# Kernel tuning notes

Hardware: AMD Instinct MI355X
Metric: run time of the kernel (lower is better)

Reference implementation:

```python
import jax, jax.numpy as jnp
import numpy as np

EPS = 1e-12  # VERY_SMALL_NUMBER
LN_EPS = 1e-5
N, NFEAT, NHID, A, P, HOPS = 50000, 256, 128, 32, 4, 2


def setup_inputs() -> dict:
    key = jax.random.key(0)
    ks = jax.random.split(key, 16)
    def w(i, shape, scale=0.05):
        return jax.random.normal(ks[i], shape, dtype=jnp.float32) * scale
    return {
        "x": jax.random.normal(ks[0], (N, NFEAT), dtype=jnp.float32),
        # input_mapper: Linear(nfeat,nhid) -> ReLU -> Linear(nhid,nhid)
        "im_w1": w(1, (NFEAT, NHID)), "im_b1": jnp.zeros((NHID,), jnp.float32),
        "im_w2": w(2, (NHID, NHID)),  "im_b2": jnp.zeros((NHID,), jnp.float32),
        # AnchorGraphLearner
        "anchors": w(3, (A, NHID), 1.0),
        "ml_w1": w(4, (P, 2 * NHID, NHID)), "ml_b1": jnp.zeros((P, NHID), jnp.float32),
        "ml_w2": w(5, (P, NHID)),            "ml_b2": jnp.zeros((P,), jnp.float32),
        # AnchorGNNLayer weights (xavier in torch; scaled randn here)
        "enc_w": w(6, (HOPS, NHID, NHID)), "enc_b": jnp.zeros((HOPS, NHID), jnp.float32),
        # LayerNorm
        "ln_g": jnp.ones((NHID,), jnp.float32), "ln_b": jnp.zeros((NHID,), jnp.float32),
        # classifier: Linear -> PReLU(nhid) -> Linear(nhid,2)
        "cls_w1": w(7, (NHID, NHID)), "cls_b1": jnp.zeros((NHID,), jnp.float32),
        "prelu_a": jnp.full((NHID,), 0.25, jnp.float32),
        "cls_w2": w(8, (NHID, 2)),   "cls_b2": jnp.zeros((2,), jnp.float32),
    }


def _forward(x, im_w1, im_b1, im_w2, im_b2, anchors, ml_w1, ml_b1, ml_w2, ml_b2,
             enc_w, enc_b, ln_g, ln_b, cls_w1, cls_b1, prelu_a, cls_w2, cls_b2):
    nhid = im_w2.shape[-1]
    # input_mapper (dropout is identity in eval)
    h = jnp.maximum(x @ im_w1 + im_b1, 0.0) @ im_w2 + im_b2  # [N, nhid]
    x_loc = h

    # --- AnchorGraphLearner: fused form of cat([x_i, a_j]) @ W1 ---
    Wx, Wa = ml_w1[:, :nhid, :], ml_w1[:, nhid:, :]  # each [P, nhid, nhid]
    attn = jnp.zeros((h.shape[0], anchors.shape[0]), h.dtype)
    for p in range(ml_w1.shape[0]):  # small fixed head count
        hx = h @ Wx[p]                               # [N, nhid]
        ha = anchors @ Wa[p]                         # [A, nhid]
        hid = jnp.maximum(hx[:, None, :] + ha[None, :, :] + ml_b1[p], 0.0)  # [N, A, nhid]
        attn = attn + jax.nn.sigmoid(hid @ ml_w2[p] + ml_b2[p])            # [N, A]
    adj = attn / ml_w1.shape[0]  # mean over heads, [N, A]

    # --- AnchorGNNLayer stack (anchor_mp normalized double matmul) ---
    node_norm = adj / jnp.maximum(adj.sum(axis=0, keepdims=True), EPS)     # col-normalized [N, A]
    anchor_norm = adj / jnp.maximum(adj.sum(axis=1, keepdims=True), EPS)   # row-normalized [N, A]
    xc = h
    for i in range(enc_w.shape[0]):
        support = xc @ enc_w[i]                          # [N, nhid]
        agg = node_norm.T @ support                      # [A, nhid]
        xc = jnp.maximum(anchor_norm @ agg + enc_b[i], 0.0)

    # residual + LayerNorm
    z = xc + x_loc
    mu = z.mean(axis=-1, keepdims=True)
    var = ((z - mu) ** 2).mean(axis=-1, keepdims=True)
    z = (z - mu) * jax.lax.rsqrt(var + LN_EPS) * ln_g + ln_b

    def classifier(t):
        t1 = t @ cls_w1 + cls_b1
        t1 = jnp.where(t1 > 0, t1, prelu_a * t1)  # PReLU(nhid)
        return t1 @ cls_w2 + cls_b2

    pred = classifier(z)                 # [N, 2]
    anchor_logits = classifier(anchors)  # [A, 2]
    anchor_vec = anchors[None]           # [1, A, nhid] (matches unsqueeze(0))
    return (pred, z, anchor_vec, anchor_logits)


def reference(x, im_w1, im_b1, im_w2, im_b2, anchors, ml_w1, ml_b1, ml_w2, ml_b2,
              enc_w, enc_b, ln_g, ln_b, cls_w1, cls_b1, prelu_a, cls_w2, cls_b2):
    return _forward(x, im_w1, im_b1, im_w2, im_b2, anchors, ml_w1, ml_b1, ml_w2, ml_b2,
                    enc_w, enc_b, ln_g, ln_b, cls_w1, cls_b1, prelu_a, cls_w2, cls_b2)
```

## Files before the change

kernel.cpp:

```cpp
#include <hip/hip_runtime.h>
#include <math.h>

#define NN 50000
#define FEAT 256
#define HID 128
#define NA 32
#define NP 4
#define TM 64
#define NBLK 782
#define NB2 781
#define LDA 132
#define EPSS 1e-12f
#define LN_EPS 1e-5f

typedef unsigned short u16;
typedef __attribute__((ext_vector_type(8))) short bf16x8;
typedef __attribute__((ext_vector_type(4))) float f32x4;

#define ADJ_F   0
#define RS_F    1600000
#define CS_F    1650000
#define AGG0_F  1650032
#define AGG1_F  1654128
#define HB_F    1658256
#define FLAG_F  1674640
#define F_END   1674672
#define XC_U   (2 * F_END)
#define SUP_U  (XC_U + NN * HID)
#define PW_U   (SUP_U + NN * HID)
#define PW_TOT 165638
#define WS_NEED_BYTES ((size_t)(PW_U + PW_TOT) * 2ULL)
#define CSP_OFF 0

#define PK_IMW1T  0
#define PK_IMW2T  32768
#define PK_MLW1T  49152
#define PK_ENCWT  114688
#define PK_CLSW1T 147456
#define PK_IMB1   163840
#define PK_IMB2   163968
#define PK_MLW2   164096
#define PK_ENCB   164608
#define PK_LNG    164864
#define PK_LNB    164992
#define PK_CLSB1  165120
#define PK_PRELU  165248
#define PK_CLSW2  165376
#define PK_CLSB2  165632
#define PK_MLB2   165634
#define PK_TOTAL  165638

#define PRED_OFF 0
#define Z_OFF    100000
#define AV_OFF   6500000
#define AL_OFF   6504096
#define OUT_TOT  6504160

__device__ __constant__ int kNel[19] = {
    NN * FEAT, FEAT * HID, HID, HID * HID, HID, NA * HID,
    NP * 2 * HID * HID, NP * HID, NP * HID, NP, 2 * HID * HID, 2 * HID,
    HID, HID, HID * HID, HID, HID, HID * 2, 2};

#define TSEG_TOT 163840
__device__ __constant__ int tLen[9]  = {32768,16384,16384,16384,16384,16384,16384,16384,16384};
__device__ __constant__ int tDst[9]  = {PK_IMW1T,PK_IMW2T,PK_MLW1T,PK_MLW1T+16384,
                                        PK_MLW1T+32768,PK_MLW1T+49152,PK_ENCWT,
                                        PK_ENCWT+16384,PK_CLSW1T};
__device__ __constant__ int tSrcT[9] = {1,3,6,6,6,6,10,10,14};
__device__ __constant__ int tBase[9] = {0,0,0,32768,65536,98304,0,16384,0};
#define VSEG_TOT 1798
__device__ __constant__ int vLen[11] = {128,128,512,256,128,128,128,128,256,2,4};
__device__ __constant__ int vDst[11] = {PK_IMB1,PK_IMB2,PK_MLW2,PK_ENCB,PK_LNG,PK_LNB,
                                        PK_CLSB1,PK_PRELU,PK_CLSW2,PK_CLSB2,PK_MLB2};
__device__ __constant__ int vSrcT[11]= {2,4,8,11,12,13,15,16,17,18,9};

struct P19 { const void* q[19]; };

__device__ __forceinline__ float b2f(u16 u) {
    union { float f; unsigned int i; } v; v.i = ((unsigned int)u) << 16; return v.f;
}
__device__ __forceinline__ u16 f2b(float f) {
    union { float f; unsigned int i; } v; v.f = f;
    unsigned int x = v.i;
    x += 0x7fffu + ((x >> 16) & 1u);
    return (u16)(x >> 16);
}
__device__ __forceinline__ float ldf(const void* p, size_t i, int fl) {
    if (fl == 1) return ((const float*)p)[i];
    if (fl == 0) return b2f(((const u16*)p)[i]);
    return 0.f;
}

__global__ __launch_bounds__(256) void k_detect_all(P19 a, int* __restrict__ flags) {
    __shared__ int sHi[256], sE[256], sO[256];
    const int b = blockIdx.x;
    const u16* p = (const u16*)a.q[b];
    const int M = (kNel[b] < 8192) ? kNel[b] : 8192;
    int cHi = 0, cE = 0, cO = 0;
    for (int j = threadIdx.x; j < M; j += 256) {
        const u16 v = p[j];
        if (j & 1) cO += (v != 0);
        else { cE += (v != 0); cHi += (((v >> 7) & 0xFF) >= 200); }
    }
    sHi[threadIdx.x] = cHi; sE[threadIdx.x] = cE; sO[threadIdx.x] = cO;
    __syncthreads();
    for (int s = 128; s > 0; s >>= 1) {
        if (threadIdx.x < (unsigned)s) {
            sHi[threadIdx.x] += sHi[threadIdx.x + s];
            sE[threadIdx.x]  += sE[threadIdx.x + s];
            sO[threadIdx.x]  += sO[threadIdx.x + s];
        }
        __syncthreads();
    }
    if (threadIdx.x == 0) {
        int f;
        if (sE[0] == 0 && sO[0] == 0) f = 2;
        else if (sHi[0] >= 4 || sE[0] == 0) f = 1;
        else f = 0;
        flags[b] = f;
    }
}

__global__ __launch_bounds__(256) void k_convT(P19 a, const int* __restrict__ flags,
                                               u16* __restrict__ pw) {
    int idx = blockIdx.x * 256 + threadIdx.x;
    if (idx >= TSEG_TOT) return;
    int off = idx, s = 0;
    while (off >= tLen[s]) { off -= tLen[s]; ++s; }
    int n, k;
    if (s == 0) { n = off >> 8; k = off & 255; }
    else        { n = off >> 7; k = off & 127; }
    const int si = tSrcT[s];
    pw[tDst[s] + off] = f2b(ldf(a.q[si], (size_t)tBase[s] + (size_t)k * 128 + n,
                                flags[si]));
}

__global__ __launch_bounds__(256) void k_convV(P19 a, const int* __restrict__ flags,
                                               u16* __restrict__ pw) {
    for (int idx = threadIdx.x; idx < VSEG_TOT; idx += 256) {
        int off = idx, s = 0;
        while (off >= vLen[s]) { off -= vLen[s]; ++s; }
        const int si = vSrcT[s];
        pw[vDst[s] + off] = f2b(ldf(a.q[si], off, flags[si]));
    }
}

__device__ __forceinline__ void mfma_64x128(const u16* As, const u16* Bt,
                                            f32x4 acc[8], int lane, int rowBase) {
    const int lr = lane & 15, lq = lane >> 4;
#pragma unroll
    for (int kc = 0; kc < 4; ++kc) {
        bf16x8 a = *(const bf16x8*)(As + (rowBase + lr) * 136 + kc * 32 + lq * 8);
#pragma unroll
        for (int t = 0; t < 8; ++t) {
            bf16x8 b = *(const bf16x8*)(Bt + (t * 16 + lr) * 136 + kc * 32 + lq * 8);
            acc[t] = __builtin_amdgcn_mfma_f32_16x16x32_bf16(a, b, acc[t], 0, 0, 0);
        }
    }
}

__global__ __launch_bounds__(256) void k_gemm2(const void* __restrict__ A,
                                               const u16* __restrict__ pw,
                                               float* __restrict__ outh,
                                               const int* __restrict__ flags) {
    __shared__ __align__(16) u16 As[64 * 136];
    __shared__ __align__(16) u16 Bt[128 * 136];
    const int fA = flags[0];
    const int tid = threadIdx.x;
    const int row0 = blockIdx.x * TM;
    const int lane = tid & 63, wv = tid >> 6, rowBase = wv * 16;
    const int lr = lane & 15, lq = lane >> 4;
    f32x4 acc[8];
    const f32x4 z4 = {0.f, 0.f, 0.f, 0.f};
#pragma unroll
    for (int t = 0; t < 8; ++t) acc[t] = z4;

    for (int kc = 0; kc < 2; ++kc) {
        for (int i = tid; i < 64 * 32; i += 256) {
            const int m = i >> 5, k4 = (i & 31) << 2;
            const int g = row0 + m;
            ushort4 o; o.x = 0; o.y = 0; o.z = 0; o.w = 0;
            if (g < NN) {
                const size_t idx = (size_t)g * FEAT + kc * 128 + k4;
                if (fA == 1) {
                    float4 v = *(const float4*)((const float*)A + idx);
                    o.x = f2b(v.x); o.y = f2b(v.y); o.z = f2b(v.z); o.w = f2b(v.w);
                } else {
                    o = *(const ushort4*)((const u16*)A + idx);
                }
            }
            *(ushort4*)&As[m * 136 + k4] = o;
        }
        for (int i = tid; i < 128 * 32; i += 256) {
            const int n = i >> 5, k4 = (i & 31) << 2;
            *(ushort4*)&Bt[n * 136 + k4] =
                *(const ushort4*)(pw + PK_IMW1T + (size_t)n * FEAT + kc * 128 + k4);
        }
        __syncthreads();
        mfma_64x128(As, Bt, acc, lane, rowBase);
        __syncthreads();
    }
#pragma unroll
    for (int t = 0; t < 8; ++t) {
        const int col = t * 16 + lr;
        const float bv = b2f(pw[PK_IMB1 + col]);
#pragma unroll
        for (int r = 0; r < 4; ++r)
            As[(rowBase + lq * 4 + r) * 136 + col] = f2b(fmaxf(acc[t][r] + bv, 0.f));
    }
    for (int i = tid; i < 128 * 32; i += 256) {
        const int n = i >> 5, k4 = (i & 31) << 2;
        *(ushort4*)&Bt[n * 136 + k4] =
            *(const ushort4*)(pw + PK_IMW2T + (size_t)n * HID + k4);
    }
    __syncthreads();
    f32x4 acc2[8];
#pragma unroll
    for (int t = 0; t < 8; ++t) acc2[t] = z4;
    mfma_64x128(As, Bt, acc2, lane, rowBase);
#pragma unroll
    for (int t = 0; t < 8; ++t) {
        const int col = t * 16 + lr;
        const float bv = b2f(pw[PK_IMB2 + col]);
#pragma unroll
        for (int r = 0; r < 4; ++r) {
            const int g = row0 + rowBase + lq * 4 + r;
            if (g < NN) outh[(size_t)g * HID + col] = acc2[t][r] + bv;
        }
    }
}

__global__ __launch_bounds__(128) void k_pre(const void* __restrict__ anchors,
                                             const void* __restrict__ ml_w1,
                                             const void* __restrict__ ml_b1,
                                             float* __restrict__ hb,
                                             const int* __restrict__ flags) {
    __shared__ float sa[HID];
    const int fAn = flags[5], fW1 = flags[6], fB1 = flags[7];
    const int p = blockIdx.x >> 5, a = blockIdx.x & 31, k = threadIdx.x;
    sa[k] = ldf(anchors, a * HID + k, fAn);
    __syncthreads();
    float acc = ldf(ml_b1, p * HID + k, fB1);
    const size_t wbase = ((size_t)p * 2 * HID + HID) * HID + k;
#pragma unroll 4
    for (int j = 0; j < HID; ++j)
        acc += sa[j] * ldf(ml_w1, wbase + (size_t)j * HID, fW1);
    hb[p * (NA * HID) + k * NA + a] = acc;
}

__global__ __launch_bounds__(128) void k_wc(const float* __restrict__ hb,
                                            const u16* __restrict__ pw,
                                            float* __restrict__ wc) {
    __shared__ float red[128];
    const int p = blockIdx.x, tid = threadIdx.x;
    const int a = tid & 31, q = tid >> 5;
    float s = 0.f;
    for (int k = q * 32; k < q * 32 + 32; ++k)
        s += b2f(pw[PK_MLW2 + p * HID + k]) * hb[(size_t)p * (NA * HID) + k * NA + a];
    red[tid] = 0.5f * s;
    __syncthreads();
    if (tid < 32)
        wc[p * NA + tid] = red[tid] + red[tid + 32] + red[tid + 64] + red[tid + 96];
}

__global__ __launch_bounds__(256) void k_anchor(const void* __restrict__ anchors,
                                                const void* __restrict__ cls_w1,
                                                const void* __restrict__ cls_b1,
                                                const void* __restrict__ prelu_a,
                                                const void* __restrict__ cls_w2,
                                                const void* __restrict__ cls_b2,
                                                float* __restrict__ out,
                                                const int* __restrict__ flags) {
    __shared__ float sa[2][HID];
    __shared__ float st1[2][HID];
    const int fAn = flags[5], fW1 = flags[14], fB1 = flags[15];
    const int fPa = flags[16], fW2 = flags[17], fB2 = flags[18];
    const int tid = threadIdx.x;
    const int a0 = blockIdx.x * 2;
    const int half = tid >> 7, k = tid & 127;
    sa[half][k] = ldf(anchors, (a0 + half) * HID + k, fAn);
    __syncthreads();
    float acc = ldf(cls_b1, k, fB1);
#pragma unroll 4
    for (int j = 0; j < HID; ++j) acc += sa[half][j] * ldf(cls_w1, j * HID + k, fW1);
    const float pa = ldf(prelu_a, k, fPa);
    st1[half][k] = acc > 0.f ? acc : pa * acc;
    __syncthreads();
    if (tid < 4) {
        const int aa = tid >> 1, c = tid & 1;
        float s = ldf(cls_b2, c, fB2);
        for (int j = 0; j < HID; ++j) s += st1[aa][j] * ldf(cls_w2, j * 2 + c, fW2);
        out[AL_OFF + (a0 + aa) * 2 + c] = s;
    }
    if (blockIdx.x == 0) {
        for (int i = tid; i < NA * HID; i += 256)
            out[AV_OFF + i] = ldf(anchors, i, fAn);
    }
}

__global__ __launch_bounds__(256) void k_fattn(const float* __restrict__ h,
                                               const u16* __restrict__ pw,
                                               const float* __restrict__ hb,
                                               const float* __restrict__ wc,
                                               float* __restrict__ adj,
                                               float* __restrict__ rowsum,
                                               float* __restrict__ csPart) {
    __shared__ __align__(16) u16 Bt[128 * 136];
    __shared__ float hws[HID];
    __shared__ float wcs[NA];
    __shared__ float swr[4][NA];
    float* hbf = (float*)&Bt[64 * 136];
    const int tid = threadIdx.x;
    const int row0 = blockIdx.x * TM;
    const int lane = tid & 63, wv = tid >> 6, rowBase = wv * 16;
    const int lr = lane & 15, lq = lane >> 4;
    const int g = tid & 3, myrow = tid >> 2;
    const int a0 = g * 8;

    bf16x8 afr[4];
    {
        const int gr = row0 + rowBase + lr;
#pragma unroll
        for (int kc = 0; kc < 4; ++kc) {
            bf16x8 t;
            if (gr < NN) {
                const float* src = h + (size_t)gr * HID + kc * 32 + lq * 8;
                float4 v0 = *(const float4*)src;
                float4 v1 = *(const float4*)(src + 4);
                t[0] = (short)f2b(v0.x); t[1] = (short)f2b(v0.y);
                t[2] = (short)f2b(v0.z); t[3] = (short)f2b(v0.w);
                t[4] = (short)f2b(v1.x); t[5] = (short)f2b(v1.y);
                t[6] = (short)f2b(v1.z); t[7] = (short)f2b(v1.w);
            } else {
#pragma unroll
                for (int j = 0; j < 8; ++j) t[j] = 0;
            }
            afr[kc] = t;
        }
    }

    float adjacc[8];
#pragma unroll
    for (int j = 0; j < 8; ++j) adjacc[j] = 0.f;

    for (int p = 0; p < NP; ++p) {
        __syncthreads();
        for (int i = tid; i < 128 * 32; i += 256) {
            const int n = i >> 5, k4 = (i & 31) << 2;
            *(ushort4*)&Bt[n * 136 + k4] =
                *(const ushort4*)(pw + PK_MLW1T + p * 16384 + n * 128 + k4);
        }
        float4 hbreg[4];
        {
            const float4* hbp4 = (const float4*)(hb + (size_t)p * (NA * HID));
#pragma unroll
            for (int j = 0; j < 4; ++j) hbreg[j] = hbp4[tid + j * 256];
        }
        if (tid < HID) hws[tid] = 0.5f * b2f(pw[PK_MLW2 + p * HID + tid]);
        if (tid < NA) wcs[tid] = wc[p * NA + tid];
        __syncthreads();

        f32x4 acc[8];
        const f32x4 z4 = {0.f, 0.f, 0.f, 0.f};
#pragma unroll
        for (int t = 0; t < 8; ++t) acc[t] = z4;
#pragma unroll
        for (int kc = 0; kc < 4; ++kc)
#pragma unroll
            for (int t = 0; t < 8; ++t) {
                bf16x8 b = *(const bf16x8*)(Bt + (t * 16 + lr) * 136 + kc * 32 + lq * 8);
                acc[t] = __builtin_amdgcn_mfma_f32_16x16x32_bf16(afr[kc], b, acc[t], 0, 0, 0);
            }
        __syncthreads();
#pragma unroll
        for (int t = 0; t < 8; ++t)
#pragma unroll
            for (int r = 0; r < 4; ++r)
                Bt[(rowBase + lq * 4 + r) * 136 + t * 16 + lr] = f2b(acc[t][r]);
#pragma unroll
        for (int j = 0; j < 4; ++j)
            ((float4*)hbf)[tid + j * 256] = hbreg[j];
        __syncthreads();

        const float b2v = b2f(pw[PK_MLB2 + p]);
        float sabs[8], wh = 0.f;
#pragma unroll
        for (int j = 0; j < 8; ++j) sabs[j] = 0.f;

#pragma unroll 4
        for (int kp = 0; kp < 64; ++kp) {
            const unsigned hx2 = *(const unsigned*)&Bt[myrow * 136 + kp * 2];
            union { unsigned u; float f; } u0, u1;
            u0.u = hx2 << 16;
            u1.u = hx2 & 0xffff0000u;
            const float f0 = u0.f, f1 = u1.f;
            const float2 hw2 = *(const float2*)&hws[kp * 2];
            wh = fmaf(hw2.x, f0, wh);
            wh = fmaf(hw2.y, f1, wh);
            const float4 c00 = *(const float4*)&hbf[(kp * 2) * NA + a0];
            const float4 c01 = *(const float4*)&hbf[(kp * 2) * NA + a0 + 4];
            const float4 c10 = *(const float4*)&hbf[(kp * 2 + 1) * NA + a0];
            const float4 c11 = *(const float4*)&hbf[(kp * 2 + 1) * NA + a0 + 4];
            sabs[0] = fmaf(hw2.x, fabsf(f0 + c00.x), sabs[0]);
            sabs[1] = fmaf(hw2.x, fabsf(f0 + c00.y), sabs[1]);
            sabs[2] = fmaf(hw2.x, fabsf(f0 + c00.z), sabs[2]);
            sabs[3] = fmaf(hw2.x, fabsf(f0 + c00.w), sabs[3]);
            sabs[4] = fmaf(hw2.x, fabsf(f0 + c01.x), sabs[4]);
            sabs[5] = fmaf(hw2.x, fabsf(f0 + c01.y), sabs[5]);
            sabs[6] = fmaf(hw2.x, fabsf(f0 + c01.z), sabs[6]);
            sabs[7] = fmaf(hw2.x, fabsf(f0 + c01.w), sabs[7]);
            sabs[0] = fmaf(hw2.y, fabsf(f1 + c10.x), sabs[0]);
            sabs[1] = fmaf(hw2.y, fabsf(f1 + c10.y), sabs[1]);
            sabs[2] = fmaf(hw2.y, fabsf(f1 + c10.z), sabs[2]);
            sabs[3] = fmaf(hw2.y, fabsf(f1 + c10.w), sabs[3]);
            sabs[4] = fmaf(hw2.y, fabsf(f1 + c11.x), sabs[4]);
            sabs[5] = fmaf(hw2.y, fabsf(f1 + c11.y), sabs[5]);
            sabs[6] = fmaf(hw2.y, fabsf(f1 + c11.z), sabs[6]);
            sabs[7] = fmaf(hw2.y, fabsf(f1 + c11.w), sabs[7]);
        }
#pragma unroll
        for (int j = 0; j < 8; ++j) {
            const float s = wh + wcs[a0 + j] + b2v + sabs[j];
            adjacc[j] += 0.25f / (1.f + __expf(-s));
        }
    }

    const int grow = row0 + myrow;
    if (grow >= NN) {
#pragma unroll
        for (int j = 0; j < 8; ++j) adjacc[j] = 0.f;
    }
    if (grow < NN) {
        float* dst = adj + (size_t)grow * NA + a0;
        *(float4*)dst = make_float4(adjacc[0], adjacc[1], adjacc[2], adjacc[3]);
        *(float4*)(dst + 4) = make_float4(adjacc[4], adjacc[5], adjacc[6], adjacc[7]);
    }
    float rs = 0.f;
#pragma unroll
    for (int j = 0; j < 8; ++j) rs += adjacc[j];
    rs += __shfl_xor(rs, 1);
    rs += __shfl_xor(rs, 2);
    if (g == 0 && grow < NN) rowsum[grow] = rs;
#pragma unroll
    for (int st = 4; st <= 32; st <<= 1)
#pragma unroll
        for (int j = 0; j < 8; ++j) adjacc[j] += __shfl_xor(adjacc[j], st);
    if (lane < 4) {
#pragma unroll
        for (int j = 0; j < 8; ++j) swr[wv][lane * 8 + j] = adjacc[j];
    }
    __syncthreads();
    if (tid < NA)
        csPart[tid * NBLK + blockIdx.x] =
            swr[0][tid] + swr[1][tid] + swr[2][tid] + swr[3][tid];
}

__global__ __launch_bounds__(256) void k_cs_red(const float* __restrict__ csPart,
                                                float* __restrict__ colsum) {
    __shared__ float red[256];
    const int a = blockIdx.x, tid = threadIdx.x;
    float s = 0.f;
    for (int b = tid; b < NBLK; b += 256) s += csPart[a * NBLK + b];
    red[tid] = s;
    __syncthreads();
    for (int st = 128; st > 0; st >>= 1) {
        if (tid < st) red[tid] += red[tid + st];
        __syncthreads();
    }
    if (tid == 0) colsum[a] = red[0];
}

__global__ __launch_bounds__(256) void k_aggT(const float* __restrict__ adj,
                                              const float* __restrict__ h,
                                              float* __restrict__ part) {
    __shared__ float sT[TM][LDA];
    __shared__ float adjT[TM][NA + 1];
    const int tid = threadIdx.x;
    const int a0 = (tid & 15) * 2, k0 = (tid >> 4) * 8;
    float acc[2][8];
#pragma unroll
    for (int ia = 0; ia < 2; ++ia)
#pragma unroll
        for (int j = 0; j < 8; ++j) acc[ia][j] = 0.f;

    const int nt = (blockIdx.x == NB2 - 1) ? 2 : 1;
    for (int t = 0; t < nt; ++t) {
        const int row0 = (blockIdx.x + t) * TM;
        __syncthreads();
        for (int i = tid; i < TM * 32; i += 256) {
            const int m = i >> 5, k4 = (i & 31) << 2, g = row0 + m;
            float4 v = make_float4(0.f, 0.f, 0.f, 0.f);
            if (g < NN) v = *(const float4*)(h + (size_t)g * HID + k4);
            *(float4*)&sT[m][k4] = v;
        }
        for (int i = tid; i < TM * NA; i += 256) {
            const int m = i >> 5, a = i & 31, g = row0 + m;
            adjT[m][a] = (g < NN) ? adj[(size_t)g * NA + a] : 0.f;
        }
        __syncthreads();
#pragma unroll 4
        for (int n = 0; n < TM; ++n) {
            const float a0v = adjT[n][a0], a1v = adjT[n][a0 + 1];
            float4 s0 = *(const float4*)&sT[n][k0];
            float4 s1 = *(const float4*)&sT[n][k0 + 4];
            float sv[8] = {s0.x, s0.y, s0.z, s0.w, s1.x, s1.y, s1.z, s1.w};
#pragma unroll
            for (int j = 0; j < 8; ++j) {
                acc[0][j] += a0v * sv[j];
                acc[1][j] += a1v * sv[j];
            }
        }
    }
    float* dst = part + (size_t)blockIdx.x * (NA * HID);
#pragma unroll
    for (int ia = 0; ia < 2; ++ia) {
        *(float4*)&dst[(a0 + ia) * HID + k0] =
            make_float4(acc[ia][0], acc[ia][1], acc[ia][2], acc[ia][3]);
        *(float4*)&dst[(a0 + ia) * HID + k0 + 4] =
            make_float4(acc[ia][4], acc[ia][5], acc[ia][6], acc[ia][7]);
    }
}

__global__ __launch_bounds__(256) void k_Tred(const float* __restrict__ part,
                                              float* __restrict__ T) {
    __shared__ float red[256];
    const int jj = threadIdx.x & 15, bq = threadIdx.x >> 4;
    const int j = blockIdx.x * 16 + jj;
    float s = 0.f;
#pragma unroll 8
    for (int b = bq; b < NB2; b += 16) s += part[(size_t)b * (NA * HID) + j];
    red[threadIdx.x] = s;
    __syncthreads();
    if (bq == 0) {
        float t = 0.f;
#pragma unroll
        for (int q = 0; q < 16; ++q) t += red[q * 16 + jj];
        T[j] = t;
    }
}

__global__ __launch_bounds__(128) void k_small(const float* __restrict__ T,
                                               const u16* __restrict__ pw,
                                               const int hop,
                                               float* __restrict__ agg) {
    __shared__ float tr[HID];
    const int a = blockIdx.x, n = threadIdx.x;
    tr[n] = T[a * HID + n];
    __syncthreads();
    const u16* w = pw + PK_ENCWT + hop * HID * HID + n * HID;
    float s = 0.f;
#pragma unroll 4
    for (int j4 = 0; j4 < HID; j4 += 4) {
        ushort4 u = *(const ushort4*)(w + j4);
        s += tr[j4] * b2f(u.x) + tr[j4 + 1] * b2f(u.y) +
             tr[j4 + 2] * b2f(u.z) + tr[j4 + 3] * b2f(u.w);
    }
    agg[a * HID + n] = s;
}

__global__ __launch_bounds__(256) void k_e2a(const float* __restrict__ adj,
                                             const float* __restrict__ rowsum,
                                             const float* __restrict__ colsum,
                                             const float* __restrict__ agg,
                                             const u16* __restrict__ pw,
                                             float* __restrict__ part) {
    __shared__ float aggn[NA][LDA];
    __shared__ float adjT[TM][NA + 1];
    __shared__ __align__(8) u16 xcs[TM * 136];
    __shared__ float csl[NA], rsl[TM];
    const int tid = threadIdx.x;
    const int n0 = (tid & 31) * 4, m0 = (tid >> 5) * 8;
    const int a0 = (tid & 15) * 2, k0 = (tid >> 4) * 8;

    if (tid < NA) csl[tid] = fmaxf(colsum[tid], EPSS);
    __syncthreads();
    for (int i = tid; i < (NA * HID) / 4; i += 256) {
        const int a = i >> 5, k4 = (i & 31) << 2;
        float4 v = *(const float4*)(agg + a * HID + k4);
        const float inv = 1.f / csl[a];
        v.x *= inv; v.y *= inv; v.z *= inv; v.w *= inv;
        *(float4*)&aggn[a][k4] = v;
    }
    float bv[4];
#pragma unroll
    for (int j = 0; j < 4; ++j) bv[j] = b2f(pw[PK_ENCB + n0 + j]);

    float acc2[2][8];
#pragma unroll
    for (int ia = 0; ia < 2; ++ia)
#pragma unroll
        for (int j = 0; j < 8; ++j) acc2[ia][j] = 0.f;

    const int nt = (blockIdx.x == NB2 - 1) ? 2 : 1;
    for (int t = 0; t < nt; ++t) {
        const int row0 = (blockIdx.x + t) * TM;
        __syncthreads();
        for (int i = tid; i < TM * NA; i += 256) {
            const int m = i >> 5, a = i & 31, g = row0 + m;
            adjT[m][a] = (g < NN) ? adj[(size_t)g * NA + a] : 0.f;
        }
        if (tid >= 64 && tid < 128) {
            const int m = tid - 64, g = row0 + m;
            rsl[m] = (g < NN) ? 1.f / fmaxf(rowsum[g], EPSS) : 0.f;
        }
        __syncthreads();
        float acc[8][4];
#pragma unroll
        for (int i = 0; i < 8; ++i)
#pragma unroll
            for (int j = 0; j < 4; ++j) acc[i][j] = 0.f;
        for (int a = 0; a < NA; ++a) {
            float4 gv = *(const float4*)&aggn[a][n0];
            float gvv[4] = {gv.x, gv.y, gv.z, gv.w};
#pragma unroll
            for (int i = 0; i < 8; ++i) {
                const float av = adjT[m0 + i][a];
#pragma unroll
                for (int j = 0; j < 4; ++j) acc[i][j] += av * gvv[j];
            }
        }
#pragma unroll
        for (int i = 0; i < 8; ++i) {
            const float r = rsl[m0 + i];
            ushort4 o;
            o.x = f2b(fmaxf(r * acc[i][0] + bv[0], 0.f));
            o.y = f2b(fmaxf(r * acc[i][1] + bv[1], 0.f));
            o.z = f2b(fmaxf(r * acc[i][2] + bv[2], 0.f));
            o.w = f2b(fmaxf(r * acc[i][3] + bv[3], 0.f));
            *(ushort4*)&xcs[(m0 + i) * 136 + n0] = o;
        }
        __syncthreads();
#pragma unroll 4
        for (int n = 0; n < TM; ++n) {
            const float a0v = adjT[n][a0], a1v = adjT[n][a0 + 1];
            ushort4 u0 = *(const ushort4*)&xcs[n * 136 + k0];
            ushort4 u1 = *(const ushort4*)&xcs[n * 136 + k0 + 4];
            float sv[8] = {b2f(u0.x), b2f(u0.y), b2f(u0.z), b2f(u0.w),
                           b2f(u1.x), b2f(u1.y), b2f(u1.z), b2f(u1.w)};
#pragma unroll
            for (int j = 0; j < 8; ++j) {
                acc2[0][j] += a0v * sv[j];
                acc2[1][j] += a1v * sv[j];
            }
        }
    }
    float* dst = part + (size_t)blockIdx.x * (NA * HID);
#pragma unroll
    for (int ia = 0; ia < 2; ++ia) {
        *(float4*)&dst[(a0 + ia) * HID + k0] =
            make_float4(acc2[ia][0], acc2[ia][1], acc2[ia][2], acc2[ia][3]);
        *(float4*)&dst[(a0 + ia) * HID + k0 + 4] =
            make_float4(acc2[ia][4], acc2[ia][5], acc2[ia][6], acc2[ia][7]);
    }
}

__global__ __launch_bounds__(256) void k_e2f(const float* __restrict__ adj,
                                             const float* __restrict__ rowsum,
                                             const float* __restrict__ colsum,
                                             const float* __restrict__ agg,
                                             const u16* __restrict__ pw,
                                             float* __restrict__ out) {
    __shared__ __align__(16) u16 As[64 * 136];
    __shared__ __align__(16) u16 uniB[128 * 136];
    __shared__ float smu[TM], sinv[TM], sg[HID], sb[HID], w2s[2 * HID];
    __shared__ float csl[NA], rsl[TM];
    float* aggn  = (float*)As;
    float* adjTf = (float*)uniB;
    float* zT    = (float*)uniB;
    const int tid = threadIdx.x;
    const int row0 = blockIdx.x * TM;
    const int lane = tid & 63, wv = tid >> 6, rowBase = wv * 16;
    const int lr = lane & 15, lq = lane >> 4;
    const int n0 = (tid & 31) * 4, m0 = (tid >> 5) * 8;
    const float* h = out + Z_OFF;

    if (tid < NA) csl[tid] = fmaxf(colsum[tid], EPSS);
    if (tid >= 64 && tid < 128) {
        const int m = tid - 64, g = row0 + m;
        rsl[m] = (g < NN) ? 1.f / fmaxf(rowsum[g], EPSS) : 0.f;
    }
    for (int i = tid; i < TM * NA; i += 256) {
        const int m = i >> 5, a = i & 31, g = row0 + m;
        adjTf[m * (NA + 1) + a] = (g < NN) ? adj[(size_t)g * NA + a] : 0.f;
    }
    __syncthreads();
    for (int i = tid; i < (NA * HID) / 4; i += 256) {
        const int a = i >> 5, k4 = (i & 31) << 2;
        float4 v = *(const float4*)(agg + a * HID + k4);
        const float inv = 1.f / csl[a];
        v.x *= inv; v.y *= inv; v.z *= inv; v.w *= inv;
        *(float4*)&aggn[a * LDA + k4] = v;
    }
    __syncthreads();
    float acc[8][4];
#pragma unroll
    for (int i = 0; i < 8; ++i)
#pragma unroll
        for (int j = 0; j < 4; ++j) acc[i][j] = 0.f;
    for (int a = 0; a < NA; ++a) {
        float4 gv = *(const float4*)&aggn[a * LDA + n0];
        float gvv[4] = {gv.x, gv.y, gv.z, gv.w};
#pragma unroll
        for (int i = 0; i < 8; ++i) {
            const float av = adjTf[(m0 + i) * (NA + 1) + a];
#pragma unroll
            for (int j = 0; j < 4; ++j) acc[i][j] += av * gvv[j];
        }
    }
    float bv[4];
#pragma unroll
    for (int j = 0; j < 4; ++j) bv[j] = b2f(pw[PK_ENCB + HID + n0 + j]);
    float xcv[8][4];
#pragma unroll
    for (int i = 0; i < 8; ++i) {
        const float r = rsl[m0 + i];
#pragma unroll
        for (int j = 0; j < 4; ++j)
            xcv[i][j] = fmaxf(r * acc[i][j] + bv[j], 0.f);
    }
    __syncthreads();
#pragma unroll
    for (int i = 0; i < 8; ++i) {
        const int g = row0 + m0 + i;
        float4 hv = make_float4(0.f, 0.f, 0.f, 0.f);
        if (g < NN) hv = *(const float4*)(h + (size_t)g * HID + n0);
        float4 zv = make_float4(xcv[i][0] + hv.x, xcv[i][1] + hv.y,
                                xcv[i][2] + hv.z, xcv[i][3] + hv.w);
        *(float4*)&zT[(m0 + i) * 132 + n0] = zv;
    }
    if (tid < HID) { sg[tid] = b2f(pw[PK_LNG + tid]); sb[tid] = b2f(pw[PK_LNB + tid]); }
    w2s[tid] = b2f(pw[PK_CLSW2 + tid]);
    __syncthreads();
    if (tid < TM) {
        float s = 0.f;
        for (int k = 0; k < HID; ++k) s += zT[tid * 132 + k];
        const float mu = s * (1.f / HID);
        float v = 0.f;
        for (int k = 0; k < HID; ++k) { const float d = zT[tid * 132 + k] - mu; v += d * d; }
        smu[tid] = mu;
        sinv[tid] = rsqrtf(v * (1.f / HID) + LN_EPS);
    }
    __syncthreads();
    for (int i = tid; i < TM * 32; i += 256) {
        const int m = i >> 5, k4 = (i & 31) << 2, g = row0 + m;
        float4 v = *(const float4*)&zT[m * 132 + k4];
        const float mu = smu[m], inv = sinv[m];
        v.x = (v.x - mu) * inv * sg[k4 + 0] + sb[k4 + 0];
        v.y = (v.y - mu) * inv * sg[k4 + 1] + sb[k4 + 1];
        v.z = (v.z - mu) * inv * sg[k4 + 2] + sb[k4 + 2];
        v.w = (v.w - mu) * inv * sg[k4 + 3] + sb[k4 + 3];
        if (g < NN) *(float4*)&out[Z_OFF + (size_t)g * HID + k4] = v;
        ushort4 o; o.x = f2b(v.x); o.y = f2b(v.y); o.z = f2b(v.z); o.w = f2b(v.w);
        *(ushort4*)&As[m * 136 + k4] = o;
    }
    __syncthreads();
    for (int i = tid; i < 128 * 32; i += 256) {
        const int n = i >> 5, k4 = (i & 31) << 2;
        *(ushort4*)&uniB[n * 136 + k4] =
            *(const ushort4*)(pw + PK_CLSW1T + n * 128 + k4);
    }
    __syncthreads();
    f32x4 macc[8];
    const f32x4 z4 = {0.f, 0.f, 0.f, 0.f};
#pragma unroll
    for (int t = 0; t < 8; ++t) macc[t] = z4;
    mfma_64x128(As, uniB, macc, lane, rowBase);
    __syncthreads();
#pragma unroll
    for (int t = 0; t < 8; ++t) {
        const int col = t * 16 + lr;
        const float bc = b2f(pw[PK_CLSB1 + col]);
        const float pa = b2f(pw[PK_PRELU + col]);
#pragma unroll
        for (int r = 0; r < 4; ++r) {
            float v = macc[t][r] + bc;
            v = v > 0.f ? v : pa * v;
            As[(rowBase + lq * 4 + r) * 136 + col] = f2b(v);
        }
    }
    __syncthreads();
    if (tid < 128) {
        const int r = tid >> 1, c = tid & 1, g = row0 + r;
        if (g < NN) {
            float s = b2f(pw[PK_CLSB2 + c]);
            for (int k = 0; k < HID; ++k) s += b2f(As[r * 136 + k]) * w2s[k * 2 + c];
            out[PRED_OFF + (size_t)g * 2 + c] = s;
        }
    }
}

extern "C" void kernel_launch(void* const* d_in, const int* in_sizes, int n_in,
                              void* d_out, int out_size, void* d_ws, size_t ws_size,
                              hipStream_t stream) {
    const bool ok = (n_in >= 19) && (out_size == OUT_TOT) &&
                    (ws_size >= WS_NEED_BYTES) &&
                    (in_sizes[0] == NN * FEAT) && (in_sizes[6] == NP * 2 * HID * HID) &&
                    (in_sizes[10] == 2 * HID * HID) && (in_sizes[17] == HID * 2);
    if (!ok) {
        hipMemsetAsync(d_out, 0, (size_t)OUT_TOT * 4, stream);
        return;
    }

    float* ws    = (float*)d_ws;
    u16*   wsu   = (u16*)d_ws;
    float* out   = (float*)d_out;
    int*   flags = (int*)(ws + FLAG_F);
    float* hbuf  = out + Z_OFF;
    u16*   pw    = wsu + PW_U;
    float* xcf   = (float*)(wsu + XC_U);
    float* csPart = xcf + CSP_OFF;
    float* partb = (float*)(wsu + SUP_U);
    float* Tbuf  = ws + HB_F;
    float* wcv   = ws + AGG1_F;

    P19 pa;
    for (int i = 0; i < 19; ++i) pa.q[i] = d_in[i];
    k_detect_all<<<19, 256, 0, stream>>>(pa, flags);
    k_convT<<<(TSEG_TOT + 255) / 256, 256, 0, stream>>>(pa, flags, pw);
    k_convV<<<1, 256, 0, stream>>>(pa, flags, pw);

    k_pre<<<NP * NA, 128, 0, stream>>>(d_in[5], d_in[6], d_in[7], ws + HB_F, flags);
    k_wc<<<NP, 128, 0, stream>>>(ws + HB_F, pw, wcv);
    k_anchor<<<NA / 2, 256, 0, stream>>>(d_in[5], d_in[14], d_in[15], d_in[16],
                                         d_in[17], d_in[18], out, flags);

    k_gemm2<<<NBLK, 256, 0, stream>>>(d_in[0], pw, hbuf, flags);

    k_fattn<<<NBLK, 256, 0, stream>>>(hbuf, pw, ws + HB_F, wcv, ws + ADJ_F,
                                      ws + RS_F, csPart);
    k_cs_red<<<NA, 256, 0, stream>>>(csPart, ws + CS_F);

    k_aggT<<<NB2, 256, 0, stream>>>(ws + ADJ_F, hbuf, partb);
    k_Tred<<<256, 256, 0, stream>>>(partb, Tbuf);
    k_small<<<NA, 128, 0, stream>>>(Tbuf, pw, 0, ws + AGG0_F);
    k_e2a<<<NB2, 256, 0, stream>>>(ws + ADJ_F, ws + RS_F, ws + CS_F, ws + AGG0_F,
                                   pw, partb);
    k_Tred<<<256, 256, 0, stream>>>(partb, Tbuf);
    k_small<<<NA, 128, 0, stream>>>(Tbuf, pw, 1, ws + AGG1_F);
    k_e2f<<<NBLK, 256, 0, stream>>>(ws + ADJ_F, ws + RS_F, ws + CS_F, ws + AGG1_F,
                                    pw, out);
}
```

Before: 446.4 us.

## Fuse adjacency-transpose aggregation into attention kernel and drop separate aggT pass

The adj^T·h partial aggregation is now computed at the end of k_fattn. It reuses the bf16 h fragments already held in registers and the adjacency values already computed, staged through shared memory, so the separate k_aggT kernel no longer re-reads adj and h from global memory. The hb buffer prefetch is moved from registers to a direct global-to-LDS copy after the MFMA phase, which lowers register pressure. k_e2a and k_Tred now use one 64-row tile per block over 782 blocks instead of giving the last block two tiles. The fused aggregation uses bf16-rounded h where k_aggT used fp32 h, which slightly changes precision, and it adds tail work and a barrier to the attention kernel.

```diff
diff --git a/kernel.cpp b/kernel.cpp
--- a/kernel.cpp
+++ b/kernel.cpp
@@ -8,7 +8,6 @@
 #define NP 4
 #define TM 64
 #define NBLK 782
-#define NB2 781
 #define LDA 132
 #define EPSS 1e-12f
 #define LN_EPS 1e-5f
@@ -30,7 +29,6 @@
 #define PW_U   (SUP_U + NN * HID)
 #define PW_TOT 165638
 #define WS_NEED_BYTES ((size_t)(PW_U + PW_TOT) * 2ULL)
-#define CSP_OFF 0
 
 #define PK_IMW1T  0
 #define PK_IMW2T  32768
@@ -304,7 +302,8 @@
                                                const float* __restrict__ wc,
                                                float* __restrict__ adj,
                                                float* __restrict__ rowsum,
-                                               float* __restrict__ csPart) {
+                                               float* __restrict__ csPart,
+                                               float* __restrict__ part) {
     __shared__ __align__(16) u16 Bt[128 * 136];
     __shared__ float hws[HID];
     __shared__ float wcs[NA];
@@ -350,12 +349,6 @@
             *(ushort4*)&Bt[n * 136 + k4] =
                 *(const ushort4*)(pw + PK_MLW1T + p * 16384 + n * 128 + k4);
         }
-        float4 hbreg[4];
-        {
-            const float4* hbp4 = (const float4*)(hb + (size_t)p * (NA * HID));
-#pragma unroll
-            for (int j = 0; j < 4; ++j) hbreg[j] = hbp4[tid + j * 256];
-        }
         if (tid < HID) hws[tid] = 0.5f * b2f(pw[PK_MLW2 + p * HID + tid]);
         if (tid < NA) wcs[tid] = wc[p * NA + tid];
         __syncthreads();
@@ -377,9 +370,12 @@
 #pragma unroll
             for (int r = 0; r < 4; ++r)
                 Bt[(rowBase + lq * 4 + r) * 136 + t * 16 + lr] = f2b(acc[t][r]);
-#pragma unroll
-        for (int j = 0; j < 4; ++j)
-            ((float4*)hbf)[tid + j * 256] = hbreg[j];
+        {
+            const float4* hbp4 = (const float4*)(hb + (size_t)p * (NA * HID));
+#pragma unroll
+            for (int j = 0; j < 4; ++j)
+                ((float4*)hbf)[tid + j * 256] = hbp4[tid + j * 256];
+        }
         __syncthreads();
 
         const float b2v = b2f(pw[PK_MLB2 + p]);
@@ -441,6 +437,14 @@
     rs += __shfl_xor(rs, 1);
     rs += __shfl_xor(rs, 2);
     if (g == 0 && grow < NN) rowsum[grow] = rs;
+    __syncthreads();
+#pragma unroll
+    for (int kc = 0; kc < 4; ++kc)
+        *(bf16x8*)&Bt[(rowBase + lr) * 136 + kc * 32 + lq * 8] = afr[kc];
+    float* adjTe = (float*)&Bt[64 * 136];
+#pragma unroll
+    for (int j = 0; j < 8; ++j)
+        adjTe[myrow * 33 + a0 + j] = adjacc[j];
 #pragma unroll
     for (int st = 4; st <= 32; st <<= 1)
 #pragma unroll
@@ -453,6 +457,33 @@
     if (tid < NA)
         csPart[tid * NBLK + blockIdx.x] =
             swr[0][tid] + swr[1][tid] + swr[2][tid] + swr[3][tid];
+    const int aA = (tid & 15) * 2, kA = (tid >> 4) * 8;
+    float acc2[2][8];
+#pragma unroll
+    for (int ia = 0; ia < 2; ++ia)
+#pragma unroll
+        for (int j = 0; j < 8; ++j) acc2[ia][j] = 0.f;
+#pragma unroll 4
+    for (int n = 0; n < TM; ++n) {
+        const float a0v = adjTe[n * 33 + aA], a1v = adjTe[n * 33 + aA + 1];
+        ushort4 u0 = *(const ushort4*)&Bt[n * 136 + kA];
+        ushort4 u1 = *(const ushort4*)&Bt[n * 136 + kA + 4];
+        float sv[8] = {b2f(u0.x), b2f(u0.y), b2f(u0.z), b2f(u0.w),
+                       b2f(u1.x), b2f(u1.y), b2f(u1.z), b2f(u1.w)};
+#pragma unroll
+        for (int j = 0; j < 8; ++j) {
+            acc2[0][j] += a0v * sv[j];
+            acc2[1][j] += a1v * sv[j];
+        }
+    }
+    float* pdst = part + (size_t)blockIdx.x * (NA * HID);
+#pragma unroll
+    for (int ia = 0; ia < 2; ++ia) {
+        *(float4*)&pdst[(aA + ia) * HID + kA] =
+            make_float4(acc2[ia][0], acc2[ia][1], acc2[ia][2], acc2[ia][3]);
+        *(float4*)&pdst[(aA + ia) * HID + kA + 4] =
+            make_float4(acc2[ia][4], acc2[ia][5], acc2[ia][6], acc2[ia][7]);
+    }
 }
 
 __global__ __launch_bounds__(256) void k_cs_red(const float* __restrict__ csPart,
@@ -470,57 +501,6 @@
     if (tid == 0) colsum[a] = red[0];
 }
 
-__global__ __launch_bounds__(256) void k_aggT(const float* __restrict__ adj,
-                                              const float* __restrict__ h,
-                                              float* __restrict__ part) {
-    __shared__ float sT[TM][LDA];
-    __shared__ float adjT[TM][NA + 1];
-    const int tid = threadIdx.x;
-    const int a0 = (tid & 15) * 2, k0 = (tid >> 4) * 8;
-    float acc[2][8];
-#pragma unroll
-    for (int ia = 0; ia < 2; ++ia)
-#pragma unroll
-        for (int j = 0; j < 8; ++j) acc[ia][j] = 0.f;
-
-    const int nt = (blockIdx.x == NB2 - 1) ? 2 : 1;
-    for (int t = 0; t < nt; ++t) {
-        const int row0 = (blockIdx.x + t) * TM;
-        __syncthreads();
-        for (int i = tid; i < TM * 32; i += 256) {
-            const int m = i >> 5, k4 = (i & 31) << 2, g = row0 + m;
-            float4 v = make_float4(0.f, 0.f, 0.f, 0.f);
-            if (g < NN) v = *(const float4*)(h + (size_t)g * HID + k4);
-            *(float4*)&sT[m][k4] = v;
-        }
-        for (int i = tid; i < TM * NA; i += 256) {
-            const int m = i >> 5, a = i & 31, g = row0 + m;
-            adjT[m][a] = (g < NN) ? adj[(size_t)g * NA + a] : 0.f;
-        }
-        __syncthreads();
-#pragma unroll 4
-        for (int n = 0; n < TM; ++n) {
-            const float a0v = adjT[n][a0], a1v = adjT[n][a0 + 1];
-            float4 s0 = *(const float4*)&sT[n][k0];
-            float4 s1 = *(const float4*)&sT[n][k0 + 4];
-            float sv[8] = {s0.x, s0.y, s0.z, s0.w, s1.x, s1.y, s1.z, s1.w};
-#pragma unroll
-            for (int j = 0; j < 8; ++j) {
-                acc[0][j] += a0v * sv[j];
-                acc[1][j] += a1v * sv[j];
-            }
-        }
-    }
-    float* dst = part + (size_t)blockIdx.x * (NA * HID);
-#pragma unroll
-    for (int ia = 0; ia < 2; ++ia) {
-        *(float4*)&dst[(a0 + ia) * HID + k0] =
-            make_float4(acc[ia][0], acc[ia][1], acc[ia][2], acc[ia][3]);
-        *(float4*)&dst[(a0 + ia) * HID + k0 + 4] =
-            make_float4(acc[ia][4], acc[ia][5], acc[ia][6], acc[ia][7]);
-    }
-}
-
 __global__ __launch_bounds__(256) void k_Tred(const float* __restrict__ part,
                                               float* __restrict__ T) {
     __shared__ float red[256];
@@ -528,7 +508,7 @@
     const int j = blockIdx.x * 16 + jj;
     float s = 0.f;
 #pragma unroll 8
-    for (int b = bq; b < NB2; b += 16) s += part[(size_t)b * (NA * HID) + j];
+    for (int b = bq; b < NBLK; b += 16) s += part[(size_t)b * (NA * HID) + j];
     red[threadIdx.x] = s;
     __syncthreads();
     if (bq == 0) {
@@ -569,10 +549,19 @@
     __shared__ __align__(8) u16 xcs[TM * 136];
     __shared__ float csl[NA], rsl[TM];
     const int tid = threadIdx.x;
+    const int row0 = blockIdx.x * TM;
     const int n0 = (tid & 31) * 4, m0 = (tid >> 5) * 8;
     const int a0 = (tid & 15) * 2, k0 = (tid >> 4) * 8;
 
     if (tid < NA) csl[tid] = fmaxf(colsum[tid], EPSS);
+    if (tid >= 64 && tid < 128) {
+        const int m = tid - 64, g = row0 + m;
+        rsl[m] = (g < NN) ? 1.f / fmaxf(rowsum[g], EPSS) : 0.f;
+    }
+    for (int i = tid; i < TM * NA; i += 256) {
+        const int m = i >> 5, a = i & 31, g = row0 + m;
+        adjT[m][a] = (g < NN) ? adj[(size_t)g * NA + a] : 0.f;
+    }
     __syncthreads();
     for (int i = tid; i < (NA * HID) / 4; i += 256) {
         const int a = i >> 5, k4 = (i & 31) << 2;
@@ -584,64 +573,49 @@
     float bv[4];
 #pragma unroll
     for (int j = 0; j < 4; ++j) bv[j] = b2f(pw[PK_ENCB + n0 + j]);
-
+    __syncthreads();
+    float acc[8][4];
+#pragma unroll
+    for (int i = 0; i < 8; ++i)
+#pragma unroll
+        for (int j = 0; j < 4; ++j) acc[i][j] = 0.f;
+    for (int a = 0; a < NA; ++a) {
+        float4 gv = *(const float4*)&aggn[a][n0];
+        float gvv[4] = {gv.x, gv.y, gv.z, gv.w};
+#pragma unroll
+        for (int i = 0; i < 8; ++i) {
+            const float av = adjT[m0 + i][a];
+#pragma unroll
+            for (int j = 0; j < 4; ++j) acc[i][j] += av * gvv[j];
+        }
+    }
+#pragma unroll
+    for (int i = 0; i < 8; ++i) {
+        const float r = rsl[m0 + i];
+        ushort4 o;
+        o.x = f2b(fmaxf(r * acc[i][0] + bv[0], 0.f));
+        o.y = f2b(fmaxf(r * acc[i][1] + bv[1], 0.f));
+        o.z = f2b(fmaxf(r * acc[i][2] + bv[2], 0.f));
+        o.w = f2b(fmaxf(r * acc[i][3] + bv[3], 0.f));
+        *(ushort4*)&xcs[(m0 + i) * 136 + n0] = o;
+    }
+    __syncthreads();
     float acc2[2][8];
 #pragma unroll
     for (int ia = 0; ia < 2; ++ia)
 #pragma unroll
         for (int j = 0; j < 8; ++j) acc2[ia][j] = 0.f;
-
-    const int nt = (blockIdx.x == NB2 - 1) ? 2 : 1;
-    for (int t = 0; t < nt; ++t) {
-        const int row0 = (blockIdx.x + t) * TM;
-        __syncthreads();
-        for (int i = tid; i < TM * NA; i += 256) {
-            const int m = i >> 5, a = i & 31, g = row0 + m;
-            adjT[m][a] = (g < NN) ? adj[(size_t)g * NA + a] : 0.f;
-        }
-        if (tid >= 64 && tid < 128) {
-            const int m = tid - 64, g = row0 + m;
-            rsl[m] = (g < NN) ? 1.f / fmaxf(rowsum[g], EPSS) : 0.f;
-        }
-        __syncthreads();
-        float acc[8][4];
-#pragma unroll
-        for (int i = 0; i < 8; ++i)
-#pragma unroll
-            for (int j = 0; j < 4; ++j) acc[i][j] = 0.f;
-        for (int a = 0; a < NA; ++a) {
-            float4 gv = *(const float4*)&aggn[a][n0];
-            float gvv[4] = {gv.x, gv.y, gv.z, gv.w};
-#pragma unroll
-            for (int i = 0; i < 8; ++i) {
-                const float av = adjT[m0 + i][a];
-#pragma unroll
-                for (int j = 0; j < 4; ++j) acc[i][j] += av * gvv[j];
-            }
-        }
-#pragma unroll
-        for (int i = 0; i < 8; ++i) {
-            const float r = rsl[m0 + i];
-            ushort4 o;
-            o.x = f2b(fmaxf(r * acc[i][0] + bv[0], 0.f));
-            o.y = f2b(fmaxf(r * acc[i][1] + bv[1], 0.f));
-            o.z = f2b(fmaxf(r * acc[i][2] + bv[2], 0.f));
-            o.w = f2b(fmaxf(r * acc[i][3] + bv[3], 0.f));
-            *(ushort4*)&xcs[(m0 + i) * 136 + n0] = o;
-        }
-        __syncthreads();
 #pragma unroll 4
-        for (int n = 0; n < TM; ++n) {
-            const float a0v = adjT[n][a0], a1v = adjT[n][a0 + 1];
-            ushort4 u0 = *(const ushort4*)&xcs[n * 136 + k0];
-            ushort4 u1 = *(const ushort4*)&xcs[n * 136 + k0 + 4];
-            float sv[8] = {b2f(u0.x), b2f(u0.y), b2f(u0.z), b2f(u0.w),
-                           b2f(u1.x), b2f(u1.y), b2f(u1.z), b2f(u1.w)};
-#pragma unroll
-            for (int j = 0; j < 8; ++j) {
-                acc2[0][j] += a0v * sv[j];
-                acc2[1][j] += a1v * sv[j];
-            }
+    for (int n = 0; n < TM; ++n) {
+        const float a0v = adjT[n][a0], a1v = adjT[n][a0 + 1];
+        ushort4 u0 = *(const ushort4*)&xcs[n * 136 + k0];
+        ushort4 u1 = *(const ushort4*)&xcs[n * 136 + k0 + 4];
+        float sv[8] = {b2f(u0.x), b2f(u0.y), b2f(u0.z), b2f(u0.w),
+                       b2f(u1.x), b2f(u1.y), b2f(u1.z), b2f(u1.w)};
+#pragma unroll
+        for (int j = 0; j < 8; ++j) {
+            acc2[0][j] += a0v * sv[j];
+            acc2[1][j] += a1v * sv[j];
         }
     }
     float* dst = part + (size_t)blockIdx.x * (NA * HID);
@@ -808,8 +782,8 @@
     float* hbuf  = out + Z_OFF;
     u16*   pw    = wsu + PW_U;
     float* xcf   = (float*)(wsu + XC_U);
-    float* csPart = xcf + CSP_OFF;
-    float* partb = (float*)(wsu + SUP_U);
+    float* csPart = xcf;
+    float* partb = xcf + 32768;
     float* Tbuf  = ws + HB_F;
     float* wcv   = ws + AGG1_F;
 
@@ -827,14 +801,13 @@
     k_gemm2<<<NBLK, 256, 0, stream>>>(d_in[0], pw, hbuf, flags);
 
     k_fattn<<<NBLK, 256, 0, stream>>>(hbuf, pw, ws + HB_F, wcv, ws + ADJ_F,
-                                      ws + RS_F, csPart);
+                                      ws + RS_F, csPart, partb);
     k_cs_red<<<NA, 256, 0, stream>>>(csPart, ws + CS_F);
 
-    k_aggT<<<NB2, 256, 0, stream>>>(ws + ADJ_F, hbuf, partb);
     k_Tred<<<256, 256, 0, stream>>>(partb, Tbuf);
     k_small<<<NA, 128, 0, stream>>>(Tbuf, pw, 0, ws + AGG0_F);
-    k_e2a<<<NB2, 256, 0, stream>>>(ws + ADJ_F, ws + RS_F, ws + CS_F, ws + AGG0_F,
-                                   pw, partb);
+    k_e2a<<<NBLK, 256, 0, stream>>>(ws + ADJ_F, ws + RS_F, ws + CS_F, ws + AGG0_F,
+                                    pw, partb);
     k_Tred<<<256, 256, 0, stream>>>(partb, Tbuf);
     k_small<<<NA, 128, 0, stream>>>(Tbuf, pw, 1, ws + AGG1_F);
     k_e2f<<<NBLK, 256, 0, stream>>>(ws + ADJ_F, ws + RS_F, ws + CS_F, ws + AGG1_F,
```

New measurement: 431.8 us. -3.3%, faster.
